# Kernel optimization log

Hardware: AMD Instinct MI355X
Metric: run time of the kernel (lower is better)

Reference implementation:

```python
import jax, jax.numpy as jnp
import numpy as np

DIST = 3.0
COEFF = 10.0
NEG_SLOPE = 0.3  # keras LeakyReLU default


def _probe_points(dist=DIST):
    # fixed 26 probe offsets on a sphere of radius `dist` (from build())
    angles = np.array(
        [[j * 0.125 - 0.125, i * 0.125 + (j - 1) * 0.0625] for j in range(3) for i in range(8)]
        + [[-0.25, 0.0], [0.25, 0.0]],
        dtype=np.float32,
    ) * (2.0 * np.pi)
    a, b = angles[:, 0], angles[:, 1]
    pts = np.stack([np.sin(a), np.cos(a) * np.cos(b), np.cos(a) * np.sin(b)], axis=-1) * dist
    return jnp.asarray(pts, dtype=jnp.float32)  # (26, 3)


def setup_inputs() -> dict:
    key = jax.random.key(0)
    k1, k2, k3 = jax.random.split(key, 3)
    B, n, f = 2, 1024, 3
    m, out_feats, num_convs = 26, 6, 5
    points = jax.random.normal(k1, (B, n, 3 + f), dtype=jnp.float32)
    # per-conv Dense(m*f -> out_feats) weights/bias, stacked over num_convs
    W = jax.random.normal(k2, (num_convs, m * f, out_feats), dtype=jnp.float32) * 0.1
    b = jax.random.normal(k3, (num_convs, out_feats), dtype=jnp.float32) * 0.1
    return {"points": points, "W": W, "b": b}


def reference(points, W, b):
    B, n, df = points.shape
    d = 3
    f = df - d
    probes = _probe_points()              # (m, d)
    m = probes.shape[0]
    coords = points[..., :d]              # (B, n, d) -> centers too (l = n)
    feats = points[..., d:]               # (B, n, f)
    centers = coords
    # probes per center: (B, l, m, d)
    probes_per_center = centers[:, :, None, :] + probes[None, None, :, :]
    # delta: (B, l, m, n, d)
    delta = coords[:, None, None, :, :] - probes_per_center[:, :, :, None, :]
    sq = jnp.sum(delta * delta, axis=-1)  # (B, l, m, n)
    wgt = COEFF / (sq + COEFF)            # inverse-distance weights
    # weighted feature sum: (B, l, m, f), averaged over n
    wf = jnp.einsum('blmn,bnf->blmf', wgt, feats) / n
    x = wf.reshape(B, n, m * f)           # (B, l, m*f)
    # num_convs parallel Dense + LeakyReLU (Dropout is identity at inference)
    h = jnp.einsum('blx,kxo->blko', x, W) + b[None, None, :, :]
    h = jnp.where(h > 0, h, NEG_SLOPE * h)
    convs = h.reshape(B, n, -1)           # (B, n, num_convs*out_feats)
    return jnp.concatenate([centers, convs], axis=-1)  # (B, n, 3 + 30)
```

## Files before the change

kernel.cpp:

```cpp
#include <hip/hip_runtime.h>


#define NPTS   1024
#define COEFF  10.0f
#define NEG    0.3f

typedef float  v2f __attribute__((ext_vector_type(2)));
typedef __fp16 h2  __attribute__((ext_vector_type(2)));

#define CA 4.24264068f
#define CY 3.91968890f
#define CZ 1.62358830f

constexpr int M0[14] = {0,5, 1,4, 2,3, 7,6, 8,12, 10,14, 24,25};
constexpr int M1[12] = {16,19, 17,18, 20,23, 21,22, 9,13, 11,15};

__device__ __forceinline__ v2f pk_fma(v2f a, v2f b, v2f c) {
  v2f d;
  asm("v_pk_fma_f32 %0, %1, %2, %3" : "=v"(d) : "v"(a), "v"(b), "v"(c));
  return d;
}
__device__ __forceinline__ v2f pk_fma_n(v2f a, v2f b, v2f c) {
  v2f d;
  asm("v_pk_fma_f32 %0, %1, %2, %3 neg_lo:[1,0,0] neg_hi:[1,0,0]"
      : "=v"(d) : "v"(a), "v"(b), "v"(c));
  return d;
}
__device__ __forceinline__ v2f pk_add(v2f a, v2f b) {
  v2f d;
  asm("v_pk_add_f32 %0, %1, %2" : "=v"(d) : "v"(a), "v"(b));
  return d;
}
__device__ __forceinline__ v2f pk_sub(v2f a, v2f b) {
  v2f d;
  asm("v_pk_add_f32 %0, %1, %2 neg_lo:[0,1] neg_hi:[0,1]"
      : "=v"(d) : "v"(a), "v"(b));
  return d;
}

#define DPP_F32(x, ctrl, rm, bm, bc)                                         \
  x += __int_as_float(__builtin_amdgcn_update_dpp(                           \
      0, __float_as_int(x), ctrl, rm, bm, bc))

#define DPP_H2(x, ctrl, rm, bm, bc)                                          \
  x = x + __builtin_bit_cast(h2, __builtin_amdgcn_update_dpp(                \
      0, __builtin_bit_cast(int, x), ctrl, rm, bm, bc))

__device__ __forceinline__ h2 h2_wave_sum_to_lane63(h2 x) {
  DPP_H2(x, 0x111, 0xf, 0xf, true);
  DPP_H2(x, 0x112, 0xf, 0xf, true);
  DPP_H2(x, 0x114, 0xf, 0xe, false);
  DPP_H2(x, 0x118, 0xf, 0xc, false);
  DPP_H2(x, 0x142, 0xa, 0xf, false);
  DPP_H2(x, 0x143, 0xc, 0xf, false);
  return x;
}

__device__ __forceinline__ void rcp8_cvt(const v2f* t, h2* wp) {
  const float p0 = t[0].x * t[0].y, p1 = t[1].x * t[1].y;
  const float p2 = t[2].x * t[2].y, p3 = t[3].x * t[3].y;
  const float q01 = p0 * p1, q23 = p2 * p3;
  const float r   = __builtin_amdgcn_rcpf(q01 * q23);
  const float r01 = q23 * r, r23 = q01 * r;
  const float i0 = p1 * r01, i1 = p0 * r01;
  const float i2 = p3 * r23, i3 = p2 * r23;
  wp[0] = __builtin_amdgcn_cvt_pkrtz(t[0].y * i0, t[0].x * i0);
  wp[1] = __builtin_amdgcn_cvt_pkrtz(t[1].y * i1, t[1].x * i1);
  wp[2] = __builtin_amdgcn_cvt_pkrtz(t[2].y * i2, t[2].x * i2);
  wp[3] = __builtin_amdgcn_cvt_pkrtz(t[3].y * i3, t[3].x * i3);
}
__device__ __forceinline__ void rcp4_cvt(const v2f* t, h2* wp) {
  const float p0 = t[0].x * t[0].y, p1 = t[1].x * t[1].y;
  const float r  = __builtin_amdgcn_rcpf(p0 * p1);
  const float i0 = p1 * r, i1 = p0 * r;
  wp[0] = __builtin_amdgcn_cvt_pkrtz(t[0].y * i0, t[0].x * i0);
  wp[1] = __builtin_amdgcn_cvt_pkrtz(t[1].y * i1, t[1].x * i1);
}

template <int HALF>
__device__ void run_main(const float* __restrict__ batch, int lane,
                         v2f cxp, v2f cyp, v2f czp, float* acc) {
  constexpr int NP = HALF ? 12 : 14;
  const v2f kCA = {CA, CA}, kCY = {CY, CY}, kCZ = {CZ, CZ};
  const v2f k6 = {6.f, 6.f}, k19 = {19.f, 19.f};

  for (int it = 0; it < NPTS / 128; ++it) {
    const float* prowA = batch + (it * 128 + lane) * 6;
    const float* prowB = prowA + 64 * 6;
    const float2 a0 = *reinterpret_cast<const float2*>(prowA);
    const float2 a1 = *reinterpret_cast<const float2*>(prowA + 2);
    const float2 a2 = *reinterpret_cast<const float2*>(prowA + 4);
    const float2 b0 = *reinterpret_cast<const float2*>(prowB);
    const float2 b1 = *reinterpret_cast<const float2*>(prowB + 2);
    const float2 b2 = *reinterpret_cast<const float2*>(prowB + 4);

    const v2f dx = pk_sub(v2f{a0.x, b0.x}, cxp);
    const v2f dy = pk_sub(v2f{a0.y, b0.y}, cyp);
    const v2f dz = pk_sub(v2f{a1.x, b1.x}, czp);
    v2f base = pk_fma(dz, dz, k19);
    base = pk_fma(dy, dy, base);
    base = pk_fma(dx, dx, base);

    v2f t[NP];
    if constexpr (HALF == 0) {
      const v2f rx = pk_fma(kCA, dx, base);
      const v2f sA = pk_fma  (kCZ, dz, rx);
      const v2f sB = pk_fma_n(kCZ, dz, rx);
      const v2f sC = pk_fma_n(kCY, dz, rx);
      const v2f sD = pk_fma  (kCY, dz, rx);
      t[0]  = pk_fma_n(kCY, dy, sA);  t[1]  = pk_fma(kCY, dy, sA);
      t[2]  = pk_fma_n(kCY, dy, sB);  t[3]  = pk_fma(kCY, dy, sB);
      t[4]  = pk_fma_n(kCZ, dy, sC);  t[5]  = pk_fma(kCZ, dy, sC);
      t[6]  = pk_fma_n(kCZ, dy, sD);  t[7]  = pk_fma(kCZ, dy, sD);
      t[8]  = pk_fma_n(k6, dy, base); t[9]  = pk_fma(k6, dy, base);
      t[10] = pk_fma_n(k6, dz, base); t[11] = pk_fma(k6, dz, base);
      t[12] = pk_fma  (k6, dx, base); t[13] = pk_fma_n(k6, dx, base);
    } else {
      const v2f rx = pk_fma_n(kCA, dx, base);
      const v2f sA = pk_fma_n(kCZ, dz, rx);
      const v2f sB = pk_fma_n(kCY, dz, rx);
      const v2f sC = pk_fma  (kCZ, dz, rx);
      const v2f sD = pk_fma  (kCY, dz, rx);
      const v2f u = pk_add(dy, dz), v = pk_sub(dy, dz);
      t[0]  = pk_fma_n(kCY, dy, sA);  t[1]  = pk_fma(kCY, dy, sA);
      t[2]  = pk_fma_n(kCZ, dy, sB);  t[3]  = pk_fma(kCZ, dy, sB);
      t[4]  = pk_fma  (kCY, dy, sC);  t[5]  = pk_fma_n(kCY, dy, sC);
      t[6]  = pk_fma  (kCZ, dy, sD);  t[7]  = pk_fma_n(kCZ, dy, sD);
      t[8]  = pk_fma_n(kCA, u, base); t[9]  = pk_fma(kCA, u, base);
      t[10] = pk_fma  (kCA, v, base); t[11] = pk_fma_n(kCA, v, base);
    }

    h2 wp[NP];
    rcp8_cvt(t + 0, wp + 0);
    rcp8_cvt(t + 4, wp + 4);
    rcp8_cvt(t + 8, wp + 8);
    if constexpr (NP == 14) rcp4_cvt(t + 12, wp + 12);

    const h2 f0p = __builtin_amdgcn_cvt_pkrtz(a1.y, b1.y);
    const h2 f1p = __builtin_amdgcn_cvt_pkrtz(a2.x, b2.x);
    const h2 f2p = __builtin_amdgcn_cvt_pkrtz(a2.y, b2.y);

    #pragma unroll
    for (int j = 0; j < NP; ++j) {
      acc[j * 3 + 0] = __builtin_amdgcn_fdot2(wp[j], f0p, acc[j * 3 + 0], false);
      acc[j * 3 + 1] = __builtin_amdgcn_fdot2(wp[j], f1p, acc[j * 3 + 1], false);
      acc[j * 3 + 2] = __builtin_amdgcn_fdot2(wp[j], f2p, acc[j * 3 + 2], false);
    }
  }
}

template <int HALF>
__device__ __forceinline__ void reduce_store(float* acc, int lane, float* sx) {
  constexpr int NP = HALF ? 12 : 14;
  constexpr int NH = NP * 3 / 2;
  h2 red[NH];
  #pragma unroll
  for (int p = 0; p < NH; ++p)
    red[p] = __builtin_amdgcn_cvt_pkrtz(acc[2 * p], acc[2 * p + 1]);
  #pragma unroll
  for (int p = 0; p < NH; ++p)
    red[p] = h2_wave_sum_to_lane63(red[p]);
  if (lane == 63) {
    #pragma unroll
    for (int p = 0; p < NH; ++p) {
      const int a0 = 2 * p, a1 = 2 * p + 1;
      const int m0 = (HALF ? M1[a0 / 3] : M0[a0 / 3]);
      const int m1 = (HALF ? M1[a1 / 3] : M0[a1 / 3]);
      sx[m0 * 3 + a0 % 3] = (float)red[p].x;
      sx[m1 * 3 + a1 % 3] = (float)red[p].y;
    }
  }
}

__global__ __launch_bounds__(256, 4) void crossconv_kernel(
    const float* __restrict__ points,
    const float* __restrict__ W,
    const float* __restrict__ bias,
    float* __restrict__ out)
{
    __shared__ __align__(16) float sx[2][80];

    const int tid    = threadIdx.x;
    const int lane   = tid & 63;
    const int w      = tid >> 6;
    const int cLocal = w >> 1;
    const int half   = w & 1;
    const int G      = blockIdx.x * 2 + cLocal;

    const float* batch = points + (G >> 10) * (NPTS * 6);
    const float* crow  = points + G * 6;
    const float  cx = crow[0], cy = crow[1], cz = crow[2];
    const v2f cxp = {cx, cx}, cyp = {cy, cy}, czp = {cz, cz};

    float acc[42];
    #pragma unroll
    for (int j = 0; j < 42; ++j) acc[j] = 0.f;

    if (half == 0) run_main<0>(batch, lane, cxp, cyp, czp, acc);
    else           run_main<1>(batch, lane, cxp, cyp, czp, acc);

    if (half == 0) reduce_store<0>(acc, lane, sx[cLocal]);
    else           reduce_store<1>(acc, lane, sx[cLocal]);
    __syncthreads();

    if (half == 0) {
      const float scale = COEFF / (float)NPTS;
      float* orow = out + G * 33;
      if (lane < 30) {
        const int k = lane / 6, o = lane % 6;
        const float* Wk = W + k * (78 * 6) + o;
        float h0 = 0.f, h1 = 0.f, h2_ = 0.f, h3 = 0.f;
        const float4* sxv = reinterpret_cast<const float4*>(sx[cLocal]);
        #pragma unroll
        for (int t4 = 0; t4 < 19; ++t4) {
          const float4 v = sxv[t4];
          h0  = fmaf(v.x, Wk[(t4 * 4 + 0) * 6], h0);
          h1  = fmaf(v.y, Wk[(t4 * 4 + 1) * 6], h1);
          h2_ = fmaf(v.z, Wk[(t4 * 4 + 2) * 6], h2_);
          h3  = fmaf(v.w, Wk[(t4 * 4 + 3) * 6], h3);
        }
        const float2 vt = *reinterpret_cast<const float2*>(&sx[cLocal][76]);
        h0 = fmaf(vt.x, Wk[76 * 6], h0);
        h1 = fmaf(vt.y, Wk[77 * 6], h1);
        const float dot = (h0 + h2_) + (h1 + h3);
        float h = fmaf(dot, scale, bias[lane]);
        h = (h > 0.f) ? h : NEG * h;
        orow[3 + lane] = h;
      } else if (lane < 33) {
        orow[lane - 30] = (lane == 30) ? cx : ((lane == 31) ? cy : cz);
      }
    }
}

extern "C" void kernel_launch(void* const* d_in, const int* in_sizes, int n_in,
                              void* d_out, int out_size, void* d_ws, size_t ws_size,
                              hipStream_t stream) {
    const float* points = (const float*)d_in[0];
    const float* W      = (const float*)d_in[1];
    const float* bias   = (const float*)d_in[2];
    float* out          = (float*)d_out;
    crossconv_kernel<<<1024, 256, 0, stream>>>(points, W, bias, out);
}
```

Measured before the change: 23.82 us.

## Process two centers per wave over half the points to reuse loads

Each wave now evaluates two centers against the same loaded point rows and covers only half of the neighbour set. Two waves per center-half then split the point range, and their partial sums are added in shared memory before the dense layer. This halves global point loads per center and gives each wave more independent work. In exchange, register pressure roughly doubles (two 42-float accumulators), and the launch bound drops its occupancy hint, which may reduce waves per SIMD.

```diff
diff --git a/kernel.cpp b/kernel.cpp
--- a/kernel.cpp
+++ b/kernel.cpp
@@ -37,10 +37,6 @@
       : "=v"(d) : "v"(a), "v"(b));
   return d;
 }
-
-#define DPP_F32(x, ctrl, rm, bm, bc)                                         \
-  x += __int_as_float(__builtin_amdgcn_update_dpp(                           \
-      0, __float_as_int(x), ctrl, rm, bm, bc))
 
 #define DPP_H2(x, ctrl, rm, bm, bc)                                          \
   x = x + __builtin_bit_cast(h2, __builtin_amdgcn_update_dpp(                \
@@ -78,14 +74,70 @@
 }
 
 template <int HALF>
-__device__ void run_main(const float* __restrict__ batch, int lane,
-                         v2f cxp, v2f cyp, v2f czp, float* acc) {
+__device__ __forceinline__ void proc_center(
+    v2f pxp, v2f pyp, v2f pzp, h2 f0p, h2 f1p, h2 f2p,
+    v2f cxp, v2f cyp, v2f czp, float* acc) {
   constexpr int NP = HALF ? 12 : 14;
   const v2f kCA = {CA, CA}, kCY = {CY, CY}, kCZ = {CZ, CZ};
   const v2f k6 = {6.f, 6.f}, k19 = {19.f, 19.f};
 
-  for (int it = 0; it < NPTS / 128; ++it) {
-    const float* prowA = batch + (it * 128 + lane) * 6;
+  const v2f dx = pk_sub(pxp, cxp);
+  const v2f dy = pk_sub(pyp, cyp);
+  const v2f dz = pk_sub(pzp, czp);
+  v2f base = pk_fma(dz, dz, k19);
+  base = pk_fma(dy, dy, base);
+  base = pk_fma(dx, dx, base);
+
+  v2f t[NP];
+  if constexpr (HALF == 0) {
+    const v2f rx = pk_fma(kCA, dx, base);
+    const v2f sA = pk_fma  (kCZ, dz, rx);
+    const v2f sB = pk_fma_n(kCZ, dz, rx);
+    const v2f sC = pk_fma_n(kCY, dz, rx);
+    const v2f sD = pk_fma  (kCY, dz, rx);
+    t[0]  = pk_fma_n(kCY, dy, sA);  t[1]  = pk_fma(kCY, dy, sA);
+    t[2]  = pk_fma_n(kCY, dy, sB);  t[3]  = pk_fma(kCY, dy, sB);
+    t[4]  = pk_fma_n(kCZ, dy, sC);  t[5]  = pk_fma(kCZ, dy, sC);
+    t[6]  = pk_fma_n(kCZ, dy, sD);  t[7]  = pk_fma(kCZ, dy, sD);
+    t[8]  = pk_fma_n(k6, dy, base); t[9]  = pk_fma(k6, dy, base);
+    t[10] = pk_fma_n(k6, dz, base); t[11] = pk_fma(k6, dz, base);
+    t[12] = pk_fma  (k6, dx, base); t[13] = pk_fma_n(k6, dx, base);
+  } else {
+    const v2f rx = pk_fma_n(kCA, dx, base);
+    const v2f sA = pk_fma_n(kCZ, dz, rx);
+    const v2f sB = pk_fma_n(kCY, dz, rx);
+    const v2f sC = pk_fma  (kCZ, dz, rx);
+    const v2f sD = pk_fma  (kCY, dz, rx);
+    const v2f u = pk_add(dy, dz), v = pk_sub(dy, dz);
+    t[0]  = pk_fma_n(kCY, dy, sA);  t[1]  = pk_fma(kCY, dy, sA);
+    t[2]  = pk_fma_n(kCZ, dy, sB);  t[3]  = pk_fma(kCZ, dy, sB);
+    t[4]  = pk_fma  (kCY, dy, sC);  t[5]  = pk_fma_n(kCY, dy, sC);
+    t[6]  = pk_fma  (kCZ, dy, sD);  t[7]  = pk_fma_n(kCZ, dy, sD);
+    t[8]  = pk_fma_n(kCA, u, base); t[9]  = pk_fma(kCA, u, base);
+    t[10] = pk_fma  (kCA, v, base); t[11] = pk_fma_n(kCA, v, base);
+  }
+
+  h2 wp[NP];
+  rcp8_cvt(t + 0, wp + 0);
+  rcp8_cvt(t + 4, wp + 4);
+  rcp8_cvt(t + 8, wp + 8);
+  if constexpr (NP == 14) rcp4_cvt(t + 12, wp + 12);
+
+  #pragma unroll
+  for (int j = 0; j < NP; ++j) {
+    acc[j * 3 + 0] = __builtin_amdgcn_fdot2(wp[j], f0p, acc[j * 3 + 0], false);
+    acc[j * 3 + 1] = __builtin_amdgcn_fdot2(wp[j], f1p, acc[j * 3 + 1], false);
+    acc[j * 3 + 2] = __builtin_amdgcn_fdot2(wp[j], f2p, acc[j * 3 + 2], false);
+  }
+}
+
+template <int HALF>
+__device__ void run_main(const float* __restrict__ batch, int row0, int lane,
+                         v2f cx0, v2f cy0, v2f cz0,
+                         v2f cx1, v2f cy1, v2f cz1,
+                         float* acc0, float* acc1) {
+  for (int it = 0; it < 4; ++it) {
+    const float* prowA = batch + (row0 + it * 128 + lane) * 6;
     const float* prowB = prowA + 64 * 6;
     const float2 a0 = *reinterpret_cast<const float2*>(prowA);
     const float2 a1 = *reinterpret_cast<const float2*>(prowA + 2);
@@ -94,58 +146,15 @@
     const float2 b1 = *reinterpret_cast<const float2*>(prowB + 2);
     const float2 b2 = *reinterpret_cast<const float2*>(prowB + 4);
 
-    const v2f dx = pk_sub(v2f{a0.x, b0.x}, cxp);
-    const v2f dy = pk_sub(v2f{a0.y, b0.y}, cyp);
-    const v2f dz = pk_sub(v2f{a1.x, b1.x}, czp);
-    v2f base = pk_fma(dz, dz, k19);
-    base = pk_fma(dy, dy, base);
-    base = pk_fma(dx, dx, base);
-
-    v2f t[NP];
-    if constexpr (HALF == 0) {
-      const v2f rx = pk_fma(kCA, dx, base);
-      const v2f sA = pk_fma  (kCZ, dz, rx);
-      const v2f sB = pk_fma_n(kCZ, dz, rx);
-      const v2f sC = pk_fma_n(kCY, dz, rx);
-      const v2f sD = pk_fma  (kCY, dz, rx);
-      t[0]  = pk_fma_n(kCY, dy, sA);  t[1]  = pk_fma(kCY, dy, sA);
-      t[2]  = pk_fma_n(kCY, dy, sB);  t[3]  = pk_fma(kCY, dy, sB);
-      t[4]  = pk_fma_n(kCZ, dy, sC);  t[5]  = pk_fma(kCZ, dy, sC);
-      t[6]  = pk_fma_n(kCZ, dy, sD);  t[7]  = pk_fma(kCZ, dy, sD);
-      t[8]  = pk_fma_n(k6, dy, base); t[9]  = pk_fma(k6, dy, base);
-      t[10] = pk_fma_n(k6, dz, base); t[11] = pk_fma(k6, dz, base);
-      t[12] = pk_fma  (k6, dx, base); t[13] = pk_fma_n(k6, dx, base);
-    } else {
-      const v2f rx = pk_fma_n(kCA, dx, base);
-      const v2f sA = pk_fma_n(kCZ, dz, rx);
-      const v2f sB = pk_fma_n(kCY, dz, rx);
-      const v2f sC = pk_fma  (kCZ, dz, rx);
-      const v2f sD = pk_fma  (kCY, dz, rx);
-      const v2f u = pk_add(dy, dz), v = pk_sub(dy, dz);
-      t[0]  = pk_fma_n(kCY, dy, sA);  t[1]  = pk_fma(kCY, dy, sA);
-      t[2]  = pk_fma_n(kCZ, dy, sB);  t[3]  = pk_fma(kCZ, dy, sB);
-      t[4]  = pk_fma  (kCY, dy, sC);  t[5]  = pk_fma_n(kCY, dy, sC);
-      t[6]  = pk_fma  (kCZ, dy, sD);  t[7]  = pk_fma_n(kCZ, dy, sD);
-      t[8]  = pk_fma_n(kCA, u, base); t[9]  = pk_fma(kCA, u, base);
-      t[10] = pk_fma  (kCA, v, base); t[11] = pk_fma_n(kCA, v, base);
-    }
-
-    h2 wp[NP];
-    rcp8_cvt(t + 0, wp + 0);
-    rcp8_cvt(t + 4, wp + 4);
-    rcp8_cvt(t + 8, wp + 8);
-    if constexpr (NP == 14) rcp4_cvt(t + 12, wp + 12);
-
+    const v2f pxp = {a0.x, b0.x};
+    const v2f pyp = {a0.y, b0.y};
+    const v2f pzp = {a1.x, b1.x};
     const h2 f0p = __builtin_amdgcn_cvt_pkrtz(a1.y, b1.y);
     const h2 f1p = __builtin_amdgcn_cvt_pkrtz(a2.x, b2.x);
     const h2 f2p = __builtin_amdgcn_cvt_pkrtz(a2.y, b2.y);
 
-    #pragma unroll
-    for (int j = 0; j < NP; ++j) {
-      acc[j * 3 + 0] = __builtin_amdgcn_fdot2(wp[j], f0p, acc[j * 3 + 0], false);
-      acc[j * 3 + 1] = __builtin_amdgcn_fdot2(wp[j], f1p, acc[j * 3 + 1], false);
-      acc[j * 3 + 2] = __builtin_amdgcn_fdot2(wp[j], f2p, acc[j * 3 + 2], false);
-    }
+    proc_center<HALF>(pxp, pyp, pzp, f0p, f1p, f2p, cx0, cy0, cz0, acc0);
+    proc_center<HALF>(pxp, pyp, pzp, f0p, f1p, f2p, cx1, cy1, cz1, acc1);
   }
 }
 
@@ -172,56 +181,70 @@
   }
 }
 
-__global__ __launch_bounds__(256, 4) void crossconv_kernel(
+__global__ __launch_bounds__(256) void crossconv_kernel(
     const float* __restrict__ points,
     const float* __restrict__ W,
     const float* __restrict__ bias,
     float* __restrict__ out)
 {
-    __shared__ __align__(16) float sx[2][80];
-
-    const int tid    = threadIdx.x;
-    const int lane   = tid & 63;
-    const int w      = tid >> 6;
-    const int cLocal = w >> 1;
-    const int half   = w & 1;
-    const int G      = blockIdx.x * 2 + cLocal;
-
-    const float* batch = points + (G >> 10) * (NPTS * 6);
-    const float* crow  = points + G * 6;
-    const float  cx = crow[0], cy = crow[1], cz = crow[2];
-    const v2f cxp = {cx, cx}, cyp = {cy, cy}, czp = {cz, cz};
-
-    float acc[42];
+    __shared__ __align__(16) float sx[2][2][80];
+
+    const int tid  = threadIdx.x;
+    const int lane = tid & 63;
+    const int w    = tid >> 6;
+    const int half = w & 1;
+    const int nnH  = w >> 1;
+    const int G0   = blockIdx.x * 2;
+
+    const float* batch = points + (G0 >> 10) * (NPTS * 6);
+    const float* cr0   = points + G0 * 6;
+    const float* cr1   = cr0 + 6;
+    const float cx0 = cr0[0], cy0 = cr0[1], cz0 = cr0[2];
+    const float cx1 = cr1[0], cy1 = cr1[1], cz1 = cr1[2];
+    const v2f cx0p = {cx0, cx0}, cy0p = {cy0, cy0}, cz0p = {cz0, cz0};
+    const v2f cx1p = {cx1, cx1}, cy1p = {cy1, cy1}, cz1p = {cz1, cz1};
+    const int row0 = nnH * (NPTS / 2);
+
+    float acc0[42], acc1[42];
     #pragma unroll
-    for (int j = 0; j < 42; ++j) acc[j] = 0.f;
-
-    if (half == 0) run_main<0>(batch, lane, cxp, cyp, czp, acc);
-    else           run_main<1>(batch, lane, cxp, cyp, czp, acc);
-
-    if (half == 0) reduce_store<0>(acc, lane, sx[cLocal]);
-    else           reduce_store<1>(acc, lane, sx[cLocal]);
+    for (int j = 0; j < 42; ++j) { acc0[j] = 0.f; acc1[j] = 0.f; }
+
+    if (half == 0)
+      run_main<0>(batch, row0, lane, cx0p, cy0p, cz0p, cx1p, cy1p, cz1p, acc0, acc1);
+    else
+      run_main<1>(batch, row0, lane, cx0p, cy0p, cz0p, cx1p, cy1p, cz1p, acc0, acc1);
+
+    if (half == 0) {
+      reduce_store<0>(acc0, lane, sx[0][nnH]);
+      reduce_store<0>(acc1, lane, sx[1][nnH]);
+    } else {
+      reduce_store<1>(acc0, lane, sx[0][nnH]);
+      reduce_store<1>(acc1, lane, sx[1][nnH]);
+    }
     __syncthreads();
 
-    if (half == 0) {
+    if (w < 2) {
+      const int   c  = w;
+      const int   G  = G0 + c;
+      const float cx = c ? cx1 : cx0, cy = c ? cy1 : cy0, cz = c ? cz1 : cz0;
       const float scale = COEFF / (float)NPTS;
       float* orow = out + G * 33;
       if (lane < 30) {
         const int k = lane / 6, o = lane % 6;
         const float* Wk = W + k * (78 * 6) + o;
         float h0 = 0.f, h1 = 0.f, h2_ = 0.f, h3 = 0.f;
-        const float4* sxv = reinterpret_cast<const float4*>(sx[cLocal]);
+        const float4* s0 = reinterpret_cast<const float4*>(sx[c][0]);
+        const float4* s1 = reinterpret_cast<const float4*>(sx[c][1]);
         #pragma unroll
         for (int t4 = 0; t4 < 19; ++t4) {
-          const float4 v = sxv[t4];
-          h0  = fmaf(v.x, Wk[(t4 * 4 + 0) * 6], h0);
-          h1  = fmaf(v.y, Wk[(t4 * 4 + 1) * 6], h1);
-          h2_ = fmaf(v.z, Wk[(t4 * 4 + 2) * 6], h2_);
-          h3  = fmaf(v.w, Wk[(t4 * 4 + 3) * 6], h3);
+          const float4 va = s0[t4], vb = s1[t4];
+          h0  = fmaf(va.x + vb.x, Wk[(t4 * 4 + 0) * 6], h0);
+          h1  = fmaf(va.y + vb.y, Wk[(t4 * 4 + 1) * 6], h1);
+          h2_ = fmaf(va.z + vb.z, Wk[(t4 * 4 + 2) * 6], h2_);
+          h3  = fmaf(va.w + vb.w, Wk[(t4 * 4 + 3) * 6], h3);
         }
-        const float2 vt = *reinterpret_cast<const float2*>(&sx[cLocal][76]);
-        h0 = fmaf(vt.x, Wk[76 * 6], h0);
-        h1 = fmaf(vt.y, Wk[77 * 6], h1);
+        h0 = fmaf(sx[c][0][76] + sx[c][1][76], Wk[76 * 6], h0);
+        h1 = fmaf(sx[c][0][77] + sx[c][1][77], Wk[77 * 6], h1);
         const float dot = (h0 + h2_) + (h1 + h3);
         float h = fmaf(dot, scale, bias[lane]);
         h = (h > 0.f) ? h : NEG * h;
```

New measurement: 25.17 us. 1.06x slower.

## Stage batch points into LDS as SoA before the main loop

Applied to the files above, without the earlier changes.

Each block now cooperatively loads the whole 1024-point batch from global memory with float4 loads and transposes it into a structure-of-arrays layout in shared memory. The main loop then reads each coordinate and feature as adjacent pairs from LDS, replacing strided global float2 loads. The center coordinates also come from LDS. This adds 24 KB of shared memory per block and a barrier, which may lower occupancy and adds a staging phase per block.

```diff
diff --git a/kernel.cpp b/kernel.cpp
--- a/kernel.cpp
+++ b/kernel.cpp
@@ -37,10 +37,6 @@
       : "=v"(d) : "v"(a), "v"(b));
   return d;
 }
-
-#define DPP_F32(x, ctrl, rm, bm, bc)                                         \
-  x += __int_as_float(__builtin_amdgcn_update_dpp(                           \
-      0, __float_as_int(x), ctrl, rm, bm, bc))
 
 #define DPP_H2(x, ctrl, rm, bm, bc)                                          \
   x = x + __builtin_bit_cast(h2, __builtin_amdgcn_update_dpp(                \
@@ -78,25 +74,24 @@
 }
 
 template <int HALF>
-__device__ void run_main(const float* __restrict__ batch, int lane,
+__device__ void run_main(const float* __restrict__ soa, int lane,
                          v2f cxp, v2f cyp, v2f czp, float* acc) {
   constexpr int NP = HALF ? 12 : 14;
   const v2f kCA = {CA, CA}, kCY = {CY, CY}, kCZ = {CZ, CZ};
   const v2f k6 = {6.f, 6.f}, k19 = {19.f, 19.f};
 
-  for (int it = 0; it < NPTS / 128; ++it) {
-    const float* prowA = batch + (it * 128 + lane) * 6;
-    const float* prowB = prowA + 64 * 6;
-    const float2 a0 = *reinterpret_cast<const float2*>(prowA);
-    const float2 a1 = *reinterpret_cast<const float2*>(prowA + 2);
-    const float2 a2 = *reinterpret_cast<const float2*>(prowA + 4);
-    const float2 b0 = *reinterpret_cast<const float2*>(prowB);
-    const float2 b1 = *reinterpret_cast<const float2*>(prowB + 2);
-    const float2 b2 = *reinterpret_cast<const float2*>(prowB + 4);
-
-    const v2f dx = pk_sub(v2f{a0.x, b0.x}, cxp);
-    const v2f dy = pk_sub(v2f{a0.y, b0.y}, cyp);
-    const v2f dz = pk_sub(v2f{a1.x, b1.x}, czp);
+  for (int it = 0; it < 8; ++it) {
+    const int nb = it * 128 + 2 * lane;
+    const v2f pxp = *reinterpret_cast<const v2f*>(&soa[0 * NPTS + nb]);
+    const v2f pyp = *reinterpret_cast<const v2f*>(&soa[1 * NPTS + nb]);
+    const v2f pzp = *reinterpret_cast<const v2f*>(&soa[2 * NPTS + nb]);
+    const v2f f0v = *reinterpret_cast<const v2f*>(&soa[3 * NPTS + nb]);
+    const v2f f1v = *reinterpret_cast<const v2f*>(&soa[4 * NPTS + nb]);
+    const v2f f2v = *reinterpret_cast<const v2f*>(&soa[5 * NPTS + nb]);
+
+    const v2f dx = pk_sub(pxp, cxp);
+    const v2f dy = pk_sub(pyp, cyp);
+    const v2f dz = pk_sub(pzp, czp);
     v2f base = pk_fma(dz, dz, k19);
     base = pk_fma(dy, dy, base);
     base = pk_fma(dx, dx, base);
@@ -136,9 +131,9 @@
     rcp8_cvt(t + 8, wp + 8);
     if constexpr (NP == 14) rcp4_cvt(t + 12, wp + 12);
 
-    const h2 f0p = __builtin_amdgcn_cvt_pkrtz(a1.y, b1.y);
-    const h2 f1p = __builtin_amdgcn_cvt_pkrtz(a2.x, b2.x);
-    const h2 f2p = __builtin_amdgcn_cvt_pkrtz(a2.y, b2.y);
+    const h2 f0p = __builtin_amdgcn_cvt_pkrtz(f0v.x, f0v.y);
+    const h2 f1p = __builtin_amdgcn_cvt_pkrtz(f1v.x, f1v.y);
+    const h2 f2p = __builtin_amdgcn_cvt_pkrtz(f2v.x, f2v.y);
 
     #pragma unroll
     for (int j = 0; j < NP; ++j) {
@@ -178,6 +173,7 @@
     const float* __restrict__ bias,
     float* __restrict__ out)
 {
+    __shared__ __align__(16) float soa[6 * NPTS];
     __shared__ __align__(16) float sx[2][80];
 
     const int tid    = threadIdx.x;
@@ -188,16 +184,33 @@
     const int G      = blockIdx.x * 2 + cLocal;
 
     const float* batch = points + (G >> 10) * (NPTS * 6);
-    const float* crow  = points + G * 6;
-    const float  cx = crow[0], cy = crow[1], cz = crow[2];
+
+    {
+      const float4* src4 = reinterpret_cast<const float4*>(batch) + 6 * tid;
+      const float4 q0 = src4[0], q1 = src4[1], q2 = src4[2];
+      const float4 q3 = src4[3], q4 = src4[4], q5 = src4[5];
+      const int r = 4 * tid;
+      soa[0*NPTS + r+0] = q0.x; soa[1*NPTS + r+0] = q0.y; soa[2*NPTS + r+0] = q0.z;
+      soa[3*NPTS + r+0] = q0.w; soa[4*NPTS + r+0] = q1.x; soa[5*NPTS + r+0] = q1.y;
+      soa[0*NPTS + r+1] = q1.z; soa[1*NPTS + r+1] = q1.w; soa[2*NPTS + r+1] = q2.x;
+      soa[3*NPTS + r+1] = q2.y; soa[4*NPTS + r+1] = q2.z; soa[5*NPTS + r+1] = q2.w;
+      soa[0*NPTS + r+2] = q3.x; soa[1*NPTS + r+2] = q3.y; soa[2*NPTS + r+2] = q3.z;
+      soa[3*NPTS + r+2] = q3.w; soa[4*NPTS + r+2] = q4.x; soa[5*NPTS + r+2] = q4.y;
+      soa[0*NPTS + r+3] = q4.z; soa[1*NPTS + r+3] = q4.w; soa[2*NPTS + r+3] = q5.x;
+      soa[3*NPTS + r+3] = q5.y; soa[4*NPTS + r+3] = q5.z; soa[5*NPTS + r+3] = q5.w;
+    }
+    __syncthreads();
+
+    const int   ci = ((blockIdx.x & 511) << 1) | cLocal;
+    const float cx = soa[0*NPTS + ci], cy = soa[1*NPTS + ci], cz = soa[2*NPTS + ci];
     const v2f cxp = {cx, cx}, cyp = {cy, cy}, czp = {cz, cz};
 
     float acc[42];
     #pragma unroll
     for (int j = 0; j < 42; ++j) acc[j] = 0.f;
 
-    if (half == 0) run_main<0>(batch, lane, cxp, cyp, czp, acc);
-    else           run_main<1>(batch, lane, cxp, cyp, czp, acc);
+    if (half == 0) run_main<0>(soa, lane, cxp, cyp, czp, acc);
+    else           run_main<1>(soa, lane, cxp, cyp, czp, acc);
 
     if (half == 0) reduce_store<0>(acc, lane, sx[cLocal]);
     else           reduce_store<1>(acc, lane, sx[cLocal]);
```

Measured after the change: 21.44 us. -10.0%, faster.
